# Kernel tuning notes

Hardware: AMD Instinct MI355X
Metric: run time of the kernel (lower is better)

## Reference

```python
import jax, jax.numpy as jnp
import numpy as np

B, G, N, P, E, F, K = 8, 256, 1024, 4, 1, 256, 4
ZERO_TOL = 1e-9
INF = 1e12
ATT_SLOPE = 0.2  # leaky relu slope inside attention


def setup_inputs() -> dict:
    key = jax.random.key(0)
    ks = jax.random.split(key, 6)
    stdv = float(1.0 / np.sqrt(G * P))
    x = jax.random.normal(ks[0], (B, G, N), jnp.float32)
    mixer = jax.random.uniform(ks[1], (P, E, 2 * F), jnp.float32, -stdv, stdv)
    weight = jax.random.uniform(ks[2], (P, E, F, G), jnp.float32, -stdv, stdv)
    weight_bias = jnp.zeros((P, E, F), jnp.float32)  # reset_parameters inits to 0
    filterWeight = jax.random.uniform(ks[3], (P, F, E, K, G), jnp.float32, -stdv, stdv)
    bias = jax.random.uniform(ks[4], (F, 1), jnp.float32, -stdv, stdv)
    adj = (jax.random.uniform(ks[5], (B, E, N, N)) < 0.05).astype(jnp.float32)
    S = jnp.maximum(adj, jnp.eye(N, dtype=jnp.float32)[None, None])
    return dict(x=x, mixer=mixer, weight=weight, weight_bias=weight_bias,
                filterWeight=filterWeight, bias=bias, S=S)


def reference(x, mixer, weight, weight_bias, filterWeight, bias, S):
    # --- learnAttentionGSOBatch ---
    # Wx: [B,P,E,F,N]
    Wx = jnp.einsum('pefg,bgn->bpefn', weight, x) + weight_bias[None, :, :, :, None]
    a1 = mixer[..., :F]   # [P,E,F]
    a2 = mixer[..., F:]   # [P,E,F]
    e1 = jnp.einsum('pef,bpefn->bpen', a1, Wx)  # a1^T W x_j
    e2 = jnp.einsum('pef,bpefn->bpen', a2, Wx)  # a2^T W x_i
    # aWx[b,p,e,i,j] = e1[j] + e2[i]  (matches a1Wx + a2Wx^T broadcast)
    aWx = e1[..., None, :] + e2[..., :, None]   # [B,P,E,N,N]
    eij = jax.nn.leaky_relu(aWx, ATT_SLOPE)
    mask = (jnp.sum(jnp.abs(S), axis=1)[:, None, None] > ZERO_TOL).astype(x.dtype)  # [B,1,1,N,N]
    aij = jax.nn.softmax(eij * mask - (1.0 - mask) * INF, axis=-1) * mask  # [B,P,E,N,N]

    # --- K-hop polynomial filter ---
    xk = jnp.broadcast_to(x[:, None, None], (B, P, E, G, N))
    zs = [xk]
    for _ in range(1, K):
        xk = jnp.matmul(xk, aij)        # diffuse along attention GSO
        zs.append(xk)
    z = jnp.stack(zs, axis=3)            # [B,P,E,K,G,N]
    # h reshape [P,F,E*K*G] contracted against z reshaped [B,P,N,E*K*G]
    y = jnp.einsum('bpekgn,pfekg->bpfn', z, filterWeight) + bias  # bias [F,1] broadcasts

    # --- forward wrapper: nonlinearity (leaky_relu, default slope 0.01) + head concat ---
    y = jax.nn.leaky_relu(y)                              # [B,P,F,N]
    y = jnp.transpose(y, (0, 3, 1, 2)).reshape(B, N, P * F)
    return jnp.transpose(y, (0, 2, 1))                    # [B, P*F, N]
```

## Files before the change

### kernel.cpp

```cpp
#include <hip/hip_runtime.h>
#include <hip/hip_bf16.h>

#define B_ 8
#define G_ 256
#define N_ 1024
#define P_ 4
#define F_ 256
#define KHOP 4
#define KG_ (KHOP * G_)

typedef unsigned short ushort_t;
typedef __bf16 bf16x8 __attribute__((ext_vector_type(8)));
typedef unsigned short u16x8 __attribute__((ext_vector_type(8)));
typedef float f32x4 __attribute__((ext_vector_type(4)));

__device__ __forceinline__ unsigned short f2bf(float f) {
  union { float fl; unsigned int i; } v; v.fl = f;
  return (unsigned short)((v.i + 0x7fffu + ((v.i >> 16) & 1u)) >> 16);
}

__device__ __forceinline__ void gload_lds16(const ushort_t* g, ushort_t* l) {
  __builtin_amdgcn_global_load_lds(
      (const __attribute__((address_space(1))) void*)g,
      (__attribute__((address_space(3))) void*)l, 16, 0, 0);
}

__global__ __launch_bounds__(256) void k_prep(
    const float* __restrict__ x, const float* __restrict__ mixer,
    const float* __restrict__ weight, const float* __restrict__ wb,
    const float* __restrict__ fw, float* __restrict__ e1, float* __restrict__ e2,
    ushort_t* __restrict__ fwbf, ushort_t* __restrict__ xT,
    float* __restrict__ sumb) {
  int blk = blockIdx.x;
  int t = threadIdx.x;
  if (blk < 128) {
    __shared__ float s1[G_], s2[G_];
    __shared__ float cred[2][4];
    int bp = blk >> 2;
    int nc = blk & 3;
    int b = bp >> 2, p = bp & (P_ - 1);
    int n = nc * 256 + t;
    float acc1 = 0.f, acc2 = 0.f;
    const float* wp = weight + (size_t)p * F_ * G_ + t;
    const float* mp = mixer + p * 2 * F_;
    for (int f = 0; f < F_; ++f) {
      float wv = wp[(size_t)f * G_];
      acc1 = fmaf(mp[f], wv, acc1);
      acc2 = fmaf(mp[F_ + f], wv, acc2);
    }
    s1[t] = acc1;
    s2[t] = acc2;
    float c1p = mp[t] * wb[p * F_ + t];
    float c2p = mp[F_ + t] * wb[p * F_ + t];
#pragma unroll
    for (int mask = 1; mask < 64; mask <<= 1) {
      c1p += __shfl_xor(c1p, mask, 64);
      c2p += __shfl_xor(c2p, mask, 64);
    }
    if ((t & 63) == 0) {
      cred[0][t >> 6] = c1p;
      cred[1][t >> 6] = c2p;
    }
    __syncthreads();
    float c1 = cred[0][0] + cred[0][1] + cred[0][2] + cred[0][3];
    float c2 = cred[1][0] + cred[1][1] + cred[1][2] + cred[1][3];
    const float* xb = x + (size_t)b * G_ * N_ + n;
    float a1 = 0.f, a2 = 0.f;
#pragma unroll 8
    for (int g = 0; g < G_; ++g) {
      float xv = xb[(size_t)g * N_];
      a1 = fmaf(s1[g], xv, a1);
      a2 = fmaf(s2[g], xv, a2);
    }
    e1[(size_t)bp * N_ + n] = c1 + a1;
    e2[(size_t)bp * N_ + n] = c2 + a2;
  } else if (blk < 128 + 1024) {
    int i = (blk - 128) * 1024 + t * 4;
    float4 v = *(const float4*)&fw[i];
    ushort4 o;
    o.x = f2bf(v.x); o.y = f2bf(v.y); o.z = f2bf(v.z); o.w = f2bf(v.w);
    *(ushort4*)&fwbf[i] = o;
  } else if (blk < 1152 + 512) {
    __shared__ ushort_t tile[64][66];
    int idx = blk - 1152;
    int n0 = (idx & 15) * 64;
    int g0 = ((idx >> 4) & 3) * 64;
    int b = idx >> 6;
    int rr = t >> 4, cc = (t & 15) * 4;
#pragma unroll
    for (int ps = 0; ps < 4; ++ps) {
      float4 v = *(const float4*)&x[((size_t)b * G_ + g0 + ps * 16 + rr) * N_ + n0 + cc];
      tile[ps * 16 + rr][cc] = f2bf(v.x);
      tile[ps * 16 + rr][cc + 1] = f2bf(v.y);
      tile[ps * 16 + rr][cc + 2] = f2bf(v.z);
      tile[ps * 16 + rr][cc + 3] = f2bf(v.w);
    }
    __syncthreads();
#pragma unroll
    for (int ps = 0; ps < 4; ++ps) {
      int nl = ps * 16 + rr;
      int gl = cc;
      ushort4 o;
      o.x = tile[gl][nl];
      o.y = tile[gl + 1][nl];
      o.z = tile[gl + 2][nl];
      o.w = tile[gl + 3][nl];
      *(ushort4*)&xT[((size_t)b * N_ + n0 + nl) * G_ + g0 + gl] = o;
    }
  } else {
    int i = (blk - 1664) * 256 + t;
    sumb[i] = 0.f;
  }
}

__global__ __launch_bounds__(256) void k_att(const float* __restrict__ e1,
                                             const float* __restrict__ e2,
                                             const float* __restrict__ S,
                                             ushort_t* __restrict__ expT,
                                             float* __restrict__ sumb) {
  __shared__ ushort_t tile[256][72];
  __shared__ float se1[256];
  __shared__ float se2[64];
  int bp = blockIdx.z;
  int b = bp >> 2;
  int i0 = blockIdx.y * 64;
  int jt = blockIdx.x;
  int j0 = jt * 256;
  int t = threadIdx.x;
  int rr = t >> 4;
  int cc4 = t & 15;
  int cc = cc4 * 4;

  se1[t] = e1[(size_t)bp * N_ + j0 + t];
  if (t < 64) se2[t] = e2[(size_t)bp * N_ + i0 + t];
  __syncthreads();

  const float* Sb = S + (size_t)b * N_ * N_;
  float re2[4];
#pragma unroll
  for (int ps = 0; ps < 4; ++ps) re2[ps] = se2[ps * 16 + rr];
  float psum[4] = {0.f, 0.f, 0.f, 0.f};
#pragma unroll
  for (int js = 0; js < 4; ++js) {
    float4 e1q = *(float4*)&se1[js * 64 + cc];
    float e1v[4] = {e1q.x, e1q.y, e1q.z, e1q.w};
#pragma unroll
    for (int ps = 0; ps < 4; ++ps) {
      int il = ps * 16 + rr;
      float4 s4 = *(const float4*)&Sb[(size_t)(i0 + il) * N_ + j0 + js * 64 + cc];
      float sv[4] = {s4.x, s4.y, s4.z, s4.w};
#pragma unroll
      for (int s = 0; s < 4; ++s) {
        float v = e1v[s] + re2[ps];
        float l = v >= 0.f ? v : 0.2f * v;
        bool m = fabsf(sv[s]) > 1e-9f;
        float e = m ? __expf(l) : 0.f;
        psum[ps] += e;
        tile[js * 64 + cc + s][il] = f2bf(e);
      }
    }
  }
#pragma unroll
  for (int mask = 1; mask < 16; mask <<= 1) {
#pragma unroll
    for (int ps = 0; ps < 4; ++ps) psum[ps] += __shfl_xor(psum[ps], mask, 64);
  }
  if (cc4 == 0) {
#pragma unroll
    for (int ps = 0; ps < 4; ++ps)
      atomicAdd(&sumb[(size_t)bp * N_ + i0 + ps * 16 + rr], psum[ps]);
  }
  __syncthreads();
  ushort_t* Tb = expT + (size_t)bp * N_ * N_;
  int jl0 = t >> 3;
  int ig = (t & 7) * 8;
#pragma unroll
  for (int pass = 0; pass < 8; ++pass) {
    int jl = pass * 32 + jl0;
    u16x8 v = *(const u16x8*)&tile[jl][ig];
    *(u16x8*)&Tb[(size_t)(j0 + jl) * N_ + i0 + ig] = v;
  }
}

__global__ __launch_bounds__(256, 2) void gemm_step(
    const ushort_t* __restrict__ Aprev, const ushort_t* __restrict__ Bt,
    const ushort_t* __restrict__ fwbf, const ushort_t* __restrict__ xT,
    const float* __restrict__ bias, const float* __restrict__ sumb,
    ushort_t* __restrict__ outb, float* __restrict__ outf,
    int kslice, int has_prev, int last) {
  __shared__ ushort_t As[2][8192];
  __shared__ ushort_t Bs[2][8192];
  int id = blockIdx.x;
  int xcd = id & 7;
  int slot = id >> 3;
  int bp = xcd * 4 + (slot >> 4);
  int inner = slot & 15;
  int m0 = (inner >> 3) * 128;
  int n0 = (inner & 7) * 128;
  int p = bp & (P_ - 1), b = bp >> 2;
  int t = threadIdx.x;
  int lane = t & 63;
  int w = t >> 6;
  int wm = w >> 1, wn = w & 1;
  int lr = lane & 15, quad = lane >> 4;

  int rowF[4], colF[4];
#pragma unroll
  for (int l = 0; l < 4; ++l) {
    int cell = l * 4 + w;
    rowF[l] = (cell >> 1) * 16 + lr;
    colF[l] = (cell & 1) * 32 + quad * 8;
  }

  const ushort_t* Abase1 = has_prev ? (Aprev + (size_t)bp * (F_ * N_)) : fwbf;
  const ushort_t* Abase2 = fwbf + (size_t)p * (F_ * KG_) + (size_t)kslice * G_;
  const ushort_t* Bbase1 = Bt + (size_t)bp * N_ * N_;
  const ushort_t* Bbase2 = xT + (size_t)b * (N_ * G_);

  const ushort_t *pA1[4], *pA2[4], *pB1[4], *pB2[4];
#pragma unroll
  for (int l = 0; l < 4; ++l) {
    pA1[l] = Abase1 + (size_t)(m0 + rowF[l]) * N_ + colF[l];
    pA2[l] = Abase2 + (size_t)(m0 + rowF[l]) * KG_ + colF[l];
    pB1[l] = Bbase1 + (size_t)(n0 + rowF[l]) * N_ + colF[l];
    pB2[l] = Bbase2 + (size_t)(n0 + rowF[l]) * G_ + colF[l];
  }

  const int ntA = has_prev ? (N_ / 64) : 0;
  const int NT = ntA + G_ / 64;

  f32x4 acc[4][4] = {};

  auto stage = [&](int it, int buf) {
    if (it < ntA) {
      int ko = it * 64;
#pragma unroll
      for (int l = 0; l < 4; ++l)
        gload_lds16(pA1[l] + ko, &As[buf][(l * 4 + w) * 512]);
#pragma unroll
      for (int l = 0; l < 4; ++l)
        gload_lds16(pB1[l] + ko, &Bs[buf][(l * 4 + w) * 512]);
    } else {
      int ko = (it - ntA) * 64;
#pragma unroll
      for (int l = 0; l < 4; ++l)
        gload_lds16(pA2[l] + ko, &As[buf][(l * 4 + w) * 512]);
#pragma unroll
      for (int l = 0; l < 4; ++l)
        gload_lds16(pB2[l] + ko, &Bs[buf][(l * 4 + w) * 512]);
    }
  };

  stage(0, 0);
  int cur = 0;
  for (int it = 0; it < NT; ++it) {
    if (it + 1 < NT) {
      stage(it + 1, cur ^ 1);
      asm volatile("s_waitcnt vmcnt(8)" ::: "memory");
    } else {
      asm volatile("s_waitcnt vmcnt(0)" ::: "memory");
    }
    __builtin_amdgcn_s_barrier();
#pragma unroll
    for (int c = 0; c < 2; ++c) {
      bf16x8 af[4], bfr[4];
#pragma unroll
      for (int mi = 0; mi < 4; ++mi)
        af[mi] = __builtin_bit_cast(bf16x8,
            *(const u16x8*)&As[cur][(((wm * 4 + mi) * 2) + c) * 512 + lane * 8]);
#pragma unroll
      for (int ni = 0; ni < 4; ++ni)
        bfr[ni] = __builtin_bit_cast(bf16x8,
            *(const u16x8*)&Bs[cur][(((wn * 4 + ni) * 2) + c) * 512 + lane * 8]);
#pragma unroll
      for (int mi = 0; mi < 4; ++mi)
#pragma unroll
        for (int ni = 0; ni < 4; ++ni)
          acc[mi][ni] = __builtin_amdgcn_mfma_f32_16x16x32_bf16(af[mi], bfr[ni], acc[mi][ni], 0, 0, 0);
    }
    __builtin_amdgcn_s_barrier();
    cur ^= 1;
  }

  if (last) {
    float* Ob = outf + (size_t)bp * (F_ * N_);
#pragma unroll
    for (int mi = 0; mi < 4; ++mi) {
      int fbase = m0 + wm * 64 + mi * 16 + quad * 4;
#pragma unroll
      for (int ni = 0; ni < 4; ++ni) {
        int n = n0 + wn * 64 + ni * 16 + lr;
#pragma unroll
        for (int r = 0; r < 4; ++r) {
          float v = acc[mi][ni][r] + bias[fbase + r];
          Ob[(size_t)(fbase + r) * N_ + n] = v >= 0.f ? v : 0.01f * v;
        }
      }
    }
  } else {
    ushort_t* Ob = outb + (size_t)bp * (F_ * N_);
    float iv[4];
#pragma unroll
    for (int ni = 0; ni < 4; ++ni)
      iv[ni] = 1.0f / sumb[(size_t)bp * N_ + n0 + wn * 64 + ni * 16 + lr];
#pragma unroll
    for (int mi = 0; mi < 4; ++mi) {
      int fbase = m0 + wm * 64 + mi * 16 + quad * 4;
#pragma unroll
      for (int ni = 0; ni < 4; ++ni) {
        int n = n0 + wn * 64 + ni * 16 + lr;
#pragma unroll
        for (int r = 0; r < 4; ++r)
          Ob[(size_t)(fbase + r) * N_ + n] = f2bf(acc[mi][ni][r] * iv[ni]);
      }
    }
  }
}

extern "C" void kernel_launch(void* const* d_in, const int* in_sizes, int n_in,
                              void* d_out, int out_size, void* d_ws, size_t ws_size,
                              hipStream_t stream) {
  const float* x = (const float*)d_in[0];
  const float* mixer = (const float*)d_in[1];
  const float* weight = (const float*)d_in[2];
  const float* wb = (const float*)d_in[3];
  const float* fw = (const float*)d_in[4];
  const float* bias = (const float*)d_in[5];
  const float* S = (const float*)d_in[6];
  float* out = (float*)d_out;

  char* ws = (char*)d_ws;
  size_t off = 0;
  auto take = [&](size_t bytes) -> char* {
    char* p = ws + off;
    off = (off + bytes + 255) & ~(size_t)255;
    return p;
  };
  float* e1 = (float*)take((size_t)B_ * P_ * N_ * 4);
  float* e2 = (float*)take((size_t)B_ * P_ * N_ * 4);
  float* sumb = (float*)take((size_t)B_ * P_ * N_ * 4);
  ushort_t* fwbf = (ushort_t*)take((size_t)P_ * F_ * KHOP * G_ * 2);
  ushort_t* xT = (ushort_t*)take((size_t)B_ * N_ * G_ * 2);
  ushort_t* expT = (ushort_t*)take((size_t)B_ * P_ * N_ * N_ * 2);
  ushort_t* sA = (ushort_t*)take((size_t)B_ * P_ * F_ * N_ * 2);
  ushort_t* sB = (ushort_t*)take((size_t)B_ * P_ * F_ * N_ * 2);

  k_prep<<<1792, 256, 0, stream>>>(x, mixer, weight, wb, fw, e1, e2, fwbf, xT, sumb);
  k_att<<<dim3(4, 16, 32), 256, 0, stream>>>(e1, e2, S, expT, sumb);

  gemm_step<<<512, 256, 0, stream>>>(nullptr, expT, fwbf, xT, bias, sumb, sA, nullptr, 3, 0, 0);
  gemm_step<<<512, 256, 0, stream>>>(sA, expT, fwbf, xT, bias, sumb, sB, nullptr, 2, 1, 0);
  gemm_step<<<512, 256, 0, stream>>>(sB, expT, fwbf, xT, bias, sumb, sA, nullptr, 1, 1, 0);
  gemm_step<<<512, 256, 0, stream>>>(sA, expT, fwbf, xT, bias, sumb, nullptr, out, 0, 1, 1);
}
```

Measured before the change: 273.3 us.

## Pre-tile GEMM operands into LDS-ready contiguous 128x64 blocks

The operands fwbf, xT, expT and the intermediate diffusion buffers are stored in a blocked layout that matches the LDS fragment order. Each GEMM stage then issues fully contiguous 16-byte global-to-LDS loads instead of strided row gathers. The intermediate bf16 outputs are staged through LDS so they can be written as contiguous tiles. This aims to improve coalescing and cut address arithmetic, at the cost of an extra LDS pass and sync in the epilogue and more complex producer kernels.

After: 226.9 us. -17.0%, faster.

```diff
diff --git a/kernel.cpp b/kernel.cpp
--- a/kernel.cpp
+++ b/kernel.cpp
@@ -8,6 +8,7 @@
 #define F_ 256
 #define KHOP 4
 #define KG_ (KHOP * G_)
+
 
 typedef unsigned short ushort_t;
 typedef __bf16 bf16x8 __attribute__((ext_vector_type(8)));
@@ -74,15 +75,29 @@
     }
     e1[(size_t)bp * N_ + n] = c1 + a1;
     e2[(size_t)bp * N_ + n] = c2 + a2;
-  } else if (blk < 128 + 1024) {
-    int i = (blk - 128) * 1024 + t * 4;
-    float4 v = *(const float4*)&fw[i];
-    ushort4 o;
-    o.x = f2bf(v.x); o.y = f2bf(v.y); o.z = f2bf(v.z); o.w = f2bf(v.w);
-    *(ushort4*)&fwbf[i] = o;
-  } else if (blk < 1152 + 512) {
+  } else if (blk < 256) {
+    int tile = blk - 128;
+    int p = tile >> 5;
+    int mb = (tile >> 4) & 1;
+    int kb = tile & 15;
+    int w = t >> 6, lane = t & 63;
+    size_t tbase = ((size_t)(p * 2 + mb) * 16 + kb) * 8192;
+#pragma unroll
+    for (int q = 0; q < 4; ++q) {
+      int cell = q * 4 + w;
+      int f = mb * 128 + (cell >> 1) * 16 + (lane & 15);
+      int kg = kb * 64 + (cell & 1) * 32 + (lane >> 4) * 8;
+      const float* s = fw + ((size_t)p * F_ + f) * KG_ + kg;
+      float4 v0 = *(const float4*)&s[0];
+      float4 v1 = *(const float4*)&s[4];
+      u16x8 o;
+      o[0] = f2bf(v0.x); o[1] = f2bf(v0.y); o[2] = f2bf(v0.z); o[3] = f2bf(v0.w);
+      o[4] = f2bf(v1.x); o[5] = f2bf(v1.y); o[6] = f2bf(v1.z); o[7] = f2bf(v1.w);
+      *(u16x8*)&fwbf[tbase + (size_t)cell * 512 + lane * 8] = o;
+    }
+  } else if (blk < 768) {
     __shared__ ushort_t tile[64][66];
-    int idx = blk - 1152;
+    int idx = blk - 256;
     int n0 = (idx & 15) * 64;
     int g0 = ((idx >> 4) & 3) * 64;
     int b = idx >> 6;
@@ -96,19 +111,24 @@
       tile[ps * 16 + rr][cc + 3] = f2bf(v.w);
     }
     __syncthreads();
-#pragma unroll
-    for (int ps = 0; ps < 4; ++ps) {
-      int nl = ps * 16 + rr;
-      int gl = cc;
-      ushort4 o;
-      o.x = tile[gl][nl];
-      o.y = tile[gl + 1][nl];
-      o.z = tile[gl + 2][nl];
-      o.w = tile[gl + 3][nl];
-      *(ushort4*)&xT[((size_t)b * N_ + n0 + nl) * G_ + g0 + gl] = o;
+    int w = t >> 6, lane = t & 63;
+    int nb = n0 >> 7;
+    int kb = g0 >> 6;
+    int rhalf = (n0 & 64) >> 4;
+    size_t tbase = ((size_t)(b * 8 + nb) * 4 + kb) * 8192;
+#pragma unroll
+    for (int q = 0; q < 2; ++q) {
+      int cl = q * 4 + w;
+      int cell = (rhalf + (cl >> 1)) * 2 + (cl & 1);
+      int nl = (cl >> 1) * 16 + (lane & 15);
+      int gl = (cl & 1) * 32 + (lane >> 4) * 8;
+      u16x8 v;
+#pragma unroll
+      for (int j = 0; j < 8; ++j) v[j] = tile[gl + j][nl];
+      *(u16x8*)&xT[tbase + (size_t)cell * 512 + lane * 8] = v;
     }
   } else {
-    int i = (blk - 1664) * 256 + t;
+    int i = (blk - 768) * 256 + t;
     sumb[i] = 0.f;
   }
 }
@@ -171,14 +191,19 @@
       atomicAdd(&sumb[(size_t)bp * N_ + i0 + ps * 16 + rr], psum[ps]);
   }
   __syncthreads();
-  ushort_t* Tb = expT + (size_t)bp * N_ * N_;
-  int jl0 = t >> 3;
-  int ig = (t & 7) * 8;
-#pragma unroll
-  for (int pass = 0; pass < 8; ++pass) {
-    int jl = pass * 32 + jl0;
-    u16x8 v = *(const u16x8*)&tile[jl][ig];
-    *(u16x8*)&Tb[(size_t)(j0 + jl) * N_ + i0 + ig] = v;
+  int w = t >> 6, lane = t & 63;
+  int kb = i0 >> 6;
+#pragma unroll
+  for (int hb = 0; hb < 2; ++hb) {
+    size_t tbase = ((size_t)(bp * 8 + (j0 >> 7) + hb) * 16 + kb) * 8192;
+#pragma unroll
+    for (int q = 0; q < 4; ++q) {
+      int cell = q * 4 + w;
+      int r = (cell >> 1) * 16 + (lane & 15);
+      int il = (cell & 1) * 32 + (lane >> 4) * 8;
+      u16x8 v = *(const u16x8*)&tile[hb * 128 + r][il];
+      *(u16x8*)&expT[tbase + (size_t)cell * 512 + lane * 8] = v;
+    }
   }
 }
 
@@ -195,8 +220,10 @@
   int slot = id >> 3;
   int bp = xcd * 4 + (slot >> 4);
   int inner = slot & 15;
-  int m0 = (inner >> 3) * 128;
-  int n0 = (inner & 7) * 128;
+  int mb = inner >> 3;
+  int m0 = mb * 128;
+  int nb = inner & 7;
+  int n0 = nb * 128;
   int p = bp & (P_ - 1), b = bp >> 2;
   int t = threadIdx.x;
   int lane = t & 63;
@@ -204,50 +231,31 @@
   int wm = w >> 1, wn = w & 1;
   int lr = lane & 15, quad = lane >> 4;
 
-  int rowF[4], colF[4];
-#pragma unroll
-  for (int l = 0; l < 4; ++l) {
-    int cell = l * 4 + w;
-    rowF[l] = (cell >> 1) * 16 + lr;
-    colF[l] = (cell & 1) * 32 + quad * 8;
-  }
-
-  const ushort_t* Abase1 = has_prev ? (Aprev + (size_t)bp * (F_ * N_)) : fwbf;
-  const ushort_t* Abase2 = fwbf + (size_t)p * (F_ * KG_) + (size_t)kslice * G_;
-  const ushort_t* Bbase1 = Bt + (size_t)bp * N_ * N_;
-  const ushort_t* Bbase2 = xT + (size_t)b * (N_ * G_);
-
-  const ushort_t *pA1[4], *pA2[4], *pB1[4], *pB2[4];
-#pragma unroll
-  for (int l = 0; l < 4; ++l) {
-    pA1[l] = Abase1 + (size_t)(m0 + rowF[l]) * N_ + colF[l];
-    pA2[l] = Abase2 + (size_t)(m0 + rowF[l]) * KG_ + colF[l];
-    pB1[l] = Bbase1 + (size_t)(n0 + rowF[l]) * N_ + colF[l];
-    pB2[l] = Bbase2 + (size_t)(n0 + rowF[l]) * G_ + colF[l];
-  }
+  const ushort_t* A1 = has_prev ? (Aprev + (size_t)(bp * 2 + mb) * 16 * 8192) : fwbf;
+  const ushort_t* A2 = fwbf + ((size_t)(p * 2 + mb) * 16 + kslice * 4) * 8192;
+  const ushort_t* B1 = Bt + (size_t)(bp * 8 + nb) * 16 * 8192;
+  const ushort_t* B2 = xT + (size_t)(b * 8 + nb) * 4 * 8192;
 
   const int ntA = has_prev ? (N_ / 64) : 0;
   const int NT = ntA + G_ / 64;
 
   f32x4 acc[4][4] = {};
 
+  int laneoff = lane * 8;
   auto stage = [&](int it, int buf) {
+    const ushort_t *Ab, *Bb;
     if (it < ntA) {
-      int ko = it * 64;
-#pragma unroll
-      for (int l = 0; l < 4; ++l)
-        gload_lds16(pA1[l] + ko, &As[buf][(l * 4 + w) * 512]);
-#pragma unroll
-      for (int l = 0; l < 4; ++l)
-        gload_lds16(pB1[l] + ko, &Bs[buf][(l * 4 + w) * 512]);
+      Ab = A1 + (size_t)it * 8192;
+      Bb = B1 + (size_t)it * 8192;
     } else {
-      int ko = (it - ntA) * 64;
-#pragma unroll
-      for (int l = 0; l < 4; ++l)
-        gload_lds16(pA2[l] + ko, &As[buf][(l * 4 + w) * 512]);
-#pragma unroll
-      for (int l = 0; l < 4; ++l)
-        gload_lds16(pB2[l] + ko, &Bs[buf][(l * 4 + w) * 512]);
+      Ab = A2 + (size_t)(it - ntA) * 8192;
+      Bb = B2 + (size_t)(it - ntA) * 8192;
+    }
+#pragma unroll
+    for (int l = 0; l < 4; ++l) {
+      int coff = (w * 4 + l) * 512;
+      gload_lds16(Ab + coff + laneoff, &As[buf][coff]);
+      gload_lds16(Bb + coff + laneoff, &Bs[buf][coff]);
     }
   };
 
@@ -298,21 +306,32 @@
       }
     }
   } else {
-    ushort_t* Ob = outb + (size_t)bp * (F_ * N_);
+    ushort_t* scratch = &As[0][0];
     float iv[4];
 #pragma unroll
     for (int ni = 0; ni < 4; ++ni)
       iv[ni] = 1.0f / sumb[(size_t)bp * N_ + n0 + wn * 64 + ni * 16 + lr];
 #pragma unroll
     for (int mi = 0; mi < 4; ++mi) {
-      int fbase = m0 + wm * 64 + mi * 16 + quad * 4;
 #pragma unroll
       for (int ni = 0; ni < 4; ++ni) {
-        int n = n0 + wn * 64 + ni * 16 + lr;
+        int nL = wn * 64 + ni * 16 + lr;
+        int kbh = nL >> 6;
+        int kloc = nL & 63;
+        int cellbase = kbh * 8192 +
+                       ((wm * 4 + mi) * 2 + (kloc >> 5)) * 512 +
+                       (((kloc >> 3) & 3) * 16 + quad * 4) * 8 + (kloc & 7);
 #pragma unroll
         for (int r = 0; r < 4; ++r)
-          Ob[(size_t)(fbase + r) * N_ + n] = f2bf(acc[mi][ni][r] * iv[ni]);
+          scratch[cellbase + r * 8] = f2bf(acc[mi][ni][r] * iv[ni]);
       }
+    }
+    __syncthreads();
+    size_t obase = ((size_t)(bp * 2 + mb) * 16 + (n0 >> 6)) * 8192;
+#pragma unroll
+    for (int pass = 0; pass < 8; ++pass) {
+      int fl = pass * 2048 + t * 8;
+      *(u16x8*)&outb[obase + fl] = *(const u16x8*)&scratch[fl];
     }
   }
 }
@@ -345,7 +364,7 @@
   ushort_t* sA = (ushort_t*)take((size_t)B_ * P_ * F_ * N_ * 2);
   ushort_t* sB = (ushort_t*)take((size_t)B_ * P_ * F_ * N_ * 2);
 
-  k_prep<<<1792, 256, 0, stream>>>(x, mixer, weight, wb, fw, e1, e2, fwbf, xT, sumb);
+  k_prep<<<896, 256, 0, stream>>>(x, mixer, weight, wb, fw, e1, e2, fwbf, xT, sumb);
   k_att<<<dim3(4, 16, 32), 256, 0, stream>>>(e1, e2, S, expT, sumb);
 
   gemm_step<<<512, 256, 0, stream>>>(nullptr, expT, fwbf, xT, bias, sumb, sA, nullptr, 3, 0, 0);
```
